# Optimization experiments

Hardware: AMD Instinct MI355X
Metric: run time of the kernel (lower is better)

The kernel has to match this reference:

```python
import jax, jax.numpy as jnp
import numpy as np
from itertools import combinations

DIM = 7
EPS = 1e-4

# --- static exterior-derivative index maps (mirrors _build_derivative_maps d2_map) ---
_IDX3 = list(combinations(range(DIM), 3))           # 35 ordered 3-form multi-indices
_POS2 = {t: i for i, t in enumerate(combinations(range(DIM), 2))}  # 21 2-form positions
_d2 = []
for _out, (i, j, k) in enumerate(_IDX3):
    for _p, (a, b, c) in enumerate([(i, j, k), (j, i, k), (k, i, j)]):
        bc = tuple(sorted((b, c)))
        s = (-1) ** _p * (1 if (b, c) == bc else -1)
        _d2.append((_out, _POS2[bc], a, s))
OUT_POS = np.array([t[0] for t in _d2], dtype=np.int32)   # (105,)
IN_POS  = np.array([t[1] for t in _d2], dtype=np.int32)   # (105,)
DCOORD  = np.array([t[2] for t in _d2], dtype=np.int32)   # (105,)
SIGNS   = np.array([t[3] for t in _d2], dtype=np.float32) # (105,)


def setup_inputs() -> dict:
    key = jax.random.key(0)
    k1, k2, k3 = jax.random.split(key, 3)
    B = 262144
    x = jax.random.normal(k1, (B, DIM), dtype=jnp.float32)
    W1 = jax.random.normal(k2, (DIM, 32), dtype=jnp.float32) * 0.3
    W2 = jax.random.normal(k3, (32, 21), dtype=jnp.float32) * 0.3
    return {"x": x, "W1": W1, "W2": W2}


def reference(x, W1, W2):
    """ExteriorDerivative.apply_2form_fd with omega_fn(x) = sin(x @ W1) @ W2.

    x: (B, 7) -> d_omega: (B, 35)
    """
    def omega_fn(xx):  # (..., 7) -> (..., 21)
        return jnp.sin(xx @ W1) @ W2

    B = x.shape[0]
    # All 7 +/- coordinate perturbations at once: (7, B, 7)
    pert = EPS * jnp.eye(DIM, dtype=x.dtype)[:, None, :]
    omega_plus = omega_fn(x[None] + pert)    # (7, B, 21)
    omega_minus = omega_fn(x[None] - pert)   # (7, B, 21)
    fd = (omega_plus - omega_minus) / (2.0 * EPS)  # central differences (7, B, 21)

    # Gather the 105 (deriv_coord, in_pos) derivative values -> (105, B)
    grads = fd[DCOORD, :, IN_POS]
    contrib = jnp.asarray(SIGNS)[:, None] * grads  # (105, B)

    # Scatter-add into the 35 3-form components (duplicate out positions accumulate)
    d_omega = jnp.zeros((B, 35), dtype=x.dtype).at[:, OUT_POS].add(contrib.T)
    return d_omega
```

## Files before the change

kernel.cpp:

```cpp
#include <hip/hip_runtime.h>

#define DIM 7
#define HD  32
#define P2  21
#define P3  35
#define BLK 256
#define NT  3
#define TPW 4

typedef __attribute__((ext_vector_type(8))) short short8v;
typedef __attribute__((ext_vector_type(4))) float float4v;

static __device__ const int TI[P3] = {
  0,0,0,0,0,0,0,0,0,0,0,0,0,0,0,
  1,1,1,1,1,1,1,1,1,1,
  2,2,2,2,2,2,
  3,3,3,
  4};
static __device__ const int TJ[P3] = {
  1,1,1,1,1, 2,2,2,2, 3,3,3, 4,4, 5,
  2,2,2,2, 3,3,3, 4,4, 5,
  3,3,3, 4,4, 5,
  4,4, 5,
  5};
static __device__ const int TK[P3] = {
  2,3,4,5,6, 3,4,5,6, 4,5,6, 5,6, 6,
  3,4,5,6, 4,5,6, 5,6, 6,
  4,5,6, 5,6, 6,
  5,6, 6,
  6};

__device__ __forceinline__ int pos2(int a, int b) {
  return a * 6 - (a * (a - 1)) / 2 + (b - a - 1);
}

__device__ __forceinline__ unsigned short f2bf(float f) {
  unsigned int u = __float_as_uint(f);
  u += 0x7fffu + ((u >> 16) & 1u);
  return (unsigned short)(u >> 16);
}
__device__ __forceinline__ float bf2f(unsigned short s) {
  return __uint_as_float(((unsigned int)s) << 16);
}

__global__ __launch_bounds__(BLK)
void dform_kernel(const float* __restrict__ x,
                  const float* __restrict__ W1,
                  const float* __restrict__ W2,
                  float* __restrict__ out, int B)
{
  __shared__ unsigned short Mhi[NT * 16 * HD];
  __shared__ unsigned short Mlo[NT * 16 * HD];

  const int tid  = threadIdx.x;
  const int lane = tid & 63;
  const int lrow = lane & 15;
  const int lgrp = lane >> 4;

  for (int idx = tid; idx < NT * 16 * HD; idx += BLK) {
    int col = idx >> 5;
    int h   = idx & (HD - 1);
    float val = 0.f;
    if (col < P3) {
      int i = TI[col], j = TJ[col], k = TK[col];
      val = W1[i * HD + h] * W2[h * P2 + pos2(j, k)]
          - W1[j * HD + h] * W2[h * P2 + pos2(i, k)]
          + W1[k * HD + h] * W2[h * P2 + pos2(i, j)];
    }
    unsigned short hs = f2bf(val);
    Mhi[idx] = hs;
    Mlo[idx] = f2bf(val - bf2f(hs));
  }

  const int h0 = lgrp * 8;
  float w1r[DIM][8];
  #pragma unroll
  for (int j = 0; j < DIM; ++j) {
    float4 p0 = *reinterpret_cast<const float4*>(&W1[j * HD + h0]);
    float4 p1 = *reinterpret_cast<const float4*>(&W1[j * HD + h0 + 4]);
    w1r[j][0] = p0.x; w1r[j][1] = p0.y; w1r[j][2] = p0.z; w1r[j][3] = p0.w;
    w1r[j][4] = p1.x; w1r[j][5] = p1.y; w1r[j][6] = p1.z; w1r[j][7] = p1.w;
  }

  __syncthreads();

  short8v bhi[NT], blo[NT];
  #pragma unroll
  for (int c = 0; c < NT; ++c) {
    int off = (c * 16 + lrow) * HD + h0;
    bhi[c] = *reinterpret_cast<const short8v*>(&Mhi[off]);
    blo[c] = *reinterpret_cast<const short8v*>(&Mlo[off]);
  }

  const int gw = blockIdx.x * (BLK / 64) + (tid >> 6);
  const int tb = gw * TPW;

  for (int i = 0; i < TPW; ++i) {
    const int t = tb + i;
    if (t * 16 >= B) break;

    int row = t * 16 + lrow;
    if (row >= B) row = B - 1;
    const int rbase = row * DIM;
    float4 a = *reinterpret_cast<const float4*>(&x[rbase]);
    float4 b = *reinterpret_cast<const float4*>(&x[rbase + 3]);
    float xr[DIM] = {a.x, a.y, a.z, a.w, b.y, b.z, b.w};

    short8v ahi, alo;
    #pragma unroll
    for (int e = 0; e < 8; ++e) {
      float tv = 0.f;
      #pragma unroll
      for (int j = 0; j < DIM; ++j) tv = fmaf(xr[j], w1r[j][e], tv);
      float cv = __cosf(tv);
      unsigned short hs = f2bf(cv);
      ahi[e] = (short)hs;
      alo[e] = (short)f2bf(cv - bf2f(hs));
    }

    float4v acc[NT];
    #pragma unroll
    for (int c = 0; c < NT; ++c) {
      acc[c][0] = 0.f; acc[c][1] = 0.f; acc[c][2] = 0.f; acc[c][3] = 0.f;
    }

    #pragma unroll
    for (int c = 0; c < NT; ++c) {
      acc[c] = __builtin_amdgcn_mfma_f32_16x16x32_bf16(ahi, bhi[c], acc[c], 0, 0, 0);
      acc[c] = __builtin_amdgcn_mfma_f32_16x16x32_bf16(ahi, blo[c], acc[c], 0, 0, 0);
      acc[c] = __builtin_amdgcn_mfma_f32_16x16x32_bf16(alo, bhi[c], acc[c], 0, 0, 0);
    }

    #pragma unroll
    for (int c = 0; c < NT; ++c) {
      const int col = c * 16 + lrow;
      #pragma unroll
      for (int r = 0; r < 4; ++r) {
        const int orow = t * 16 + lgrp * 4 + r;
        if (col < P3 && orow < B)
          out[orow * P3 + col] = acc[c][r];
      }
    }
  }
}

extern "C" void kernel_launch(void* const* d_in, const int* in_sizes, int n_in,
                              void* d_out, int out_size, void* d_ws, size_t ws_size,
                              hipStream_t stream) {
  const float* x  = (const float*)d_in[0];
  const float* W1 = (const float*)d_in[1];
  const float* W2 = (const float*)d_in[2];
  float* out = (float*)d_out;
  const int B = in_sizes[0] / DIM;
  const int ntiles = (B + 15) / 16;
  const int waves  = (ntiles + TPW - 1) / TPW;
  const int grid   = (waves + (BLK / 64) - 1) / (BLK / 64);
  hipLaunchKernelGGL(dform_kernel, dim3(grid), dim3(BLK), 0, stream,
                     x, W1, W2, out, B);
}
```

Measured before the change: 21.65 us.

## Use single fp16 MFMA, swap operands for row-wise vector stores, prefetch x

Replaces the three-pass bf16 hi/lo split MFMA with a single fp16 MFMA per tile, removing the split-conversion arithmetic and two thirds of the matrix ops. The A/B operands are swapped so each lane holds four consecutive output columns of one row, which allows float4 vector stores in place of scattered scalar stores. All TPW x rows are loaded up front so the load latency overlaps with compute. fp16 precision on the cos values and the combined weights lowers accuracy relative to the compensated bf16 scheme, and the reduced-precision products may sit near the tolerance limit.

```diff
diff --git a/kernel.cpp b/kernel.cpp
--- a/kernel.cpp
+++ b/kernel.cpp
@@ -8,8 +8,8 @@
 #define NT  3
 #define TPW 4
 
-typedef __attribute__((ext_vector_type(8))) short short8v;
-typedef __attribute__((ext_vector_type(4))) float float4v;
+typedef __attribute__((ext_vector_type(8))) _Float16 half8v;
+typedef __attribute__((ext_vector_type(4))) float  float4v;
 
 static __device__ const int TI[P3] = {
   0,0,0,0,0,0,0,0,0,0,0,0,0,0,0,
@@ -34,23 +34,13 @@
   return a * 6 - (a * (a - 1)) / 2 + (b - a - 1);
 }
 
-__device__ __forceinline__ unsigned short f2bf(float f) {
-  unsigned int u = __float_as_uint(f);
-  u += 0x7fffu + ((u >> 16) & 1u);
-  return (unsigned short)(u >> 16);
-}
-__device__ __forceinline__ float bf2f(unsigned short s) {
-  return __uint_as_float(((unsigned int)s) << 16);
-}
-
 __global__ __launch_bounds__(BLK)
 void dform_kernel(const float* __restrict__ x,
                   const float* __restrict__ W1,
                   const float* __restrict__ W2,
                   float* __restrict__ out, int B)
 {
-  __shared__ unsigned short Mhi[NT * 16 * HD];
-  __shared__ unsigned short Mlo[NT * 16 * HD];
+  __shared__ _Float16 Mh[NT * 16 * HD];
 
   const int tid  = threadIdx.x;
   const int lane = tid & 63;
@@ -67,9 +57,7 @@
           - W1[j * HD + h] * W2[h * P2 + pos2(i, k)]
           + W1[k * HD + h] * W2[h * P2 + pos2(i, j)];
     }
-    unsigned short hs = f2bf(val);
-    Mhi[idx] = hs;
-    Mlo[idx] = f2bf(val - bf2f(hs));
+    Mh[idx] = (_Float16)val;
   }
 
   const int h0 = lgrp * 8;
@@ -84,61 +72,60 @@
 
   __syncthreads();
 
-  short8v bhi[NT], blo[NT];
+  half8v mfrag[NT];
   #pragma unroll
   for (int c = 0; c < NT; ++c) {
     int off = (c * 16 + lrow) * HD + h0;
-    bhi[c] = *reinterpret_cast<const short8v*>(&Mhi[off]);
-    blo[c] = *reinterpret_cast<const short8v*>(&Mlo[off]);
+    mfrag[c] = *reinterpret_cast<const half8v*>(&Mh[off]);
   }
 
   const int gw = blockIdx.x * (BLK / 64) + (tid >> 6);
   const int tb = gw * TPW;
 
+  float xr[TPW][DIM];
+  #pragma unroll
+  for (int i = 0; i < TPW; ++i) {
+    int row = (tb + i) * 16 + lrow;
+    if (row >= B) row = B - 1;
+    const int rbase = row * DIM;
+    float4 a = *reinterpret_cast<const float4*>(&x[rbase]);
+    float4 b = *reinterpret_cast<const float4*>(&x[rbase + 3]);
+    xr[i][0] = a.x; xr[i][1] = a.y; xr[i][2] = a.z; xr[i][3] = a.w;
+    xr[i][4] = b.y; xr[i][5] = b.z; xr[i][6] = b.w;
+  }
+
+  #pragma unroll
   for (int i = 0; i < TPW; ++i) {
     const int t = tb + i;
     if (t * 16 >= B) break;
 
-    int row = t * 16 + lrow;
-    if (row >= B) row = B - 1;
-    const int rbase = row * DIM;
-    float4 a = *reinterpret_cast<const float4*>(&x[rbase]);
-    float4 b = *reinterpret_cast<const float4*>(&x[rbase + 3]);
-    float xr[DIM] = {a.x, a.y, a.z, a.w, b.y, b.z, b.w};
-
-    short8v ahi, alo;
+    half8v cfrag;
     #pragma unroll
     for (int e = 0; e < 8; ++e) {
       float tv = 0.f;
       #pragma unroll
-      for (int j = 0; j < DIM; ++j) tv = fmaf(xr[j], w1r[j][e], tv);
-      float cv = __cosf(tv);
-      unsigned short hs = f2bf(cv);
-      ahi[e] = (short)hs;
-      alo[e] = (short)f2bf(cv - bf2f(hs));
+      for (int j = 0; j < DIM; ++j) tv = fmaf(xr[i][j], w1r[j][e], tv);
+      cfrag[e] = (_Float16)__cosf(tv);
     }
 
     float4v acc[NT];
     #pragma unroll
     for (int c = 0; c < NT; ++c) {
       acc[c][0] = 0.f; acc[c][1] = 0.f; acc[c][2] = 0.f; acc[c][3] = 0.f;
+      acc[c] = __builtin_amdgcn_mfma_f32_16x16x32_f16(mfrag[c], cfrag, acc[c], 0, 0, 0);
     }
 
-    #pragma unroll
-    for (int c = 0; c < NT; ++c) {
-      acc[c] = __builtin_amdgcn_mfma_f32_16x16x32_bf16(ahi, bhi[c], acc[c], 0, 0, 0);
-      acc[c] = __builtin_amdgcn_mfma_f32_16x16x32_bf16(ahi, blo[c], acc[c], 0, 0, 0);
-      acc[c] = __builtin_amdgcn_mfma_f32_16x16x32_bf16(alo, bhi[c], acc[c], 0, 0, 0);
-    }
-
-    #pragma unroll
-    for (int c = 0; c < NT; ++c) {
-      const int col = c * 16 + lrow;
-      #pragma unroll
-      for (int r = 0; r < 4; ++r) {
-        const int orow = t * 16 + lgrp * 4 + r;
-        if (col < P3 && orow < B)
-          out[orow * P3 + col] = acc[c][r];
+    const int row = t * 16 + lrow;
+    if (row < B) {
+      float* op = out + (long long)row * P3;
+      const int cb = lgrp * 4;
+      *reinterpret_cast<float4*>(op + cb) =
+          make_float4(acc[0][0], acc[0][1], acc[0][2], acc[0][3]);
+      *reinterpret_cast<float4*>(op + 16 + cb) =
+          make_float4(acc[1][0], acc[1][1], acc[1][2], acc[1][3]);
+      if (lgrp == 0) {
+        *reinterpret_cast<float2*>(op + 32) = make_float2(acc[2][0], acc[2][1]);
+        op[34] = acc[2][2];
       }
     }
   }
```

Result: faster. 19.83 us (-8.4%).
